# Kernel tuning notes

Measured on AMD Instinct MI355X. Metric: run time of the kernel, lower is better.

Reference implementation:

```python
import jax, jax.numpy as jnp
import numpy as np

B, T, N, D, H = 8, 24, 512, 128, 8
HD = D // H
HID = int(D * 2.0)
SCALES = (1.0, 0.01)


def _l2norm(a):
    # F.normalize(dim=-1), eps=1e-12
    n = jnp.sqrt(jnp.sum(a * a, axis=-1, keepdims=True))
    return a / jnp.maximum(n, 1e-12)


def _layernorm(a, g, b):
    mu = a.mean(-1, keepdims=True)
    var = ((a - mu) ** 2).mean(-1, keepdims=True)
    return (a - mu) / jnp.sqrt(var + 1e-5) * g + b


def _fast_attention_layer(z, qkv_w, out_w, out_b):
    # z: [B,T,N,D]; qkv_w: [D,3D]; out_w: [2D,D]; out_b: [D]
    b, t, n, d = z.shape
    q, k, v = jnp.split(z @ qkv_w, 3, axis=-1)          # each [B,T,N,D]
    q = q.reshape(b, t, n, H, HD)
    k = k.reshape(b, t, n, H, HD)
    v = v.reshape(b, t, n, H, HD)
    qn = _l2norm(q)
    kn = _l2norm(k)
    # spatial linear attention (tokens = nodes, axis 2)
    kvs = jnp.einsum('btnhm,btnhd->bthmd', kn, v)
    num = jnp.einsum('btnhm,bthmd->btnhd', qn, kvs) + n * v
    den = jnp.einsum('btnhm,bthm->btnh', qn, kn.sum(axis=2))[..., None] + n
    out_s = (num / den).reshape(b, t, n, d)
    # temporal linear attention (tokens = time steps, axis 1)
    kvt = jnp.einsum('btnhm,btnhd->bnhmd', kn, v)
    numt = jnp.einsum('btnhm,bnhmd->btnhd', qn, kvt) + t * v
    dent = jnp.einsum('btnhm,bnhm->btnh', qn, kn.sum(axis=1))[..., None] + t
    out_t = (numt / dent).reshape(b, t, n, d)
    return jnp.concatenate([out_s, out_t], axis=-1) @ out_w + out_b


def setup_inputs() -> dict:
    key = jax.random.key(0)
    ks = jax.random.split(key, 20)
    s = 0.02
    inp = {
        'x': jax.random.normal(ks[0], (B, T, N, D), jnp.float32),
        'graph': jax.random.uniform(ks[1], (T, N, N), jnp.float32) / N,
        'qkv_w0': jax.random.normal(ks[2], (D, 3 * D), jnp.float32) * s,
        'out_w0': jax.random.normal(ks[3], (2 * D, D), jnp.float32) * s,
        'out_b0': jnp.zeros((D,), jnp.float32),
        'pw_w0': jax.random.normal(ks[4], (D, D), jnp.float32) * s,
        'pw_b0': jax.random.normal(ks[5], (D,), jnp.float32) * s,
        'qkv_w1': jax.random.normal(ks[6], (D, 3 * D), jnp.float32) * s,
        'out_w1': jax.random.normal(ks[7], (2 * D, D), jnp.float32) * s,
        'out_b1': jnp.zeros((D,), jnp.float32),
        'pw_w1': jax.random.normal(ks[8], (D, D), jnp.float32) * s,
        'pw_b1': jax.random.normal(ks[9], (D,), jnp.float32) * s,
        'fc1_w': jax.random.normal(ks[10], (D, HID), jnp.float32) * s,
        'fc1_b': jnp.zeros((HID,), jnp.float32),
        'fc2_w': jax.random.normal(ks[11], (HID, D), jnp.float32) * s,
        'fc2_b': jnp.zeros((D,), jnp.float32),
        'ln1_g': jnp.ones((D,), jnp.float32),
        'ln1_b': jnp.zeros((D,), jnp.float32),
        'ln2_g': jnp.ones((D,), jnp.float32),
        'ln2_b': jnp.zeros((D,), jnp.float32),
    }
    return inp


def reference(x, graph, qkv_w0, out_w0, out_b0, pw_w0, pw_b0,
              qkv_w1, out_w1, out_b1, pw_w1, pw_b1,
              fc1_w, fc1_b, fc2_w, fc2_b, ln1_g, ln1_b, ln2_g, ln2_b):
    # GraphPropagate (Ks=order=2): x_loc = [x, graph @ x]; dropout in eval mode
    x1 = jnp.einsum('tni,btid->btnd', graph, x)
    x_loc = (x, x1)
    layer_params = ((qkv_w0, out_w0, out_b0, pw_w0, pw_b0),
                    (qkv_w1, out_w1, out_b1, pw_w1, pw_b1))
    c = x
    x_glo = x
    for k in range(2):
        qkv_w, out_w, out_b, pw_w, pw_b = layer_params[k]
        att = _fast_attention_layer(x_loc[k], qkv_w, out_w, out_b)
        pw = c @ pw_w + pw_b
        x_glo = x_glo + att * pw * SCALES[k]
        c = att
    h = _layernorm(x + x_glo, ln1_g, ln1_b)
    mlp = jax.nn.relu(h @ fc1_w + fc1_b) @ fc2_w + fc2_b
    return _layernorm(h + mlp, ln2_g, ln2_b)
```

## Files before the change

### kernel.cpp

```cpp
#include <hip/hip_runtime.h>
#include <cstddef>

#define Bb 8
#define Tt 24
#define Nn 512
#define Dd 128
#define Hh 8

typedef unsigned short u16;
using short8 = __attribute__((ext_vector_type(8))) short;
using f32x4  = __attribute__((ext_vector_type(4))) float;

__device__ __forceinline__ float b2f(u16 u) {
  union { unsigned u; float f; } w; w.u = ((unsigned)u) << 16; return w.f;
}
__device__ __forceinline__ u16 f2b(float f) {
  union { float f; unsigned u; } w; w.f = f;
  unsigned r = w.u + 0x7FFFu + ((w.u >> 16) & 1u);
  return (u16)(r >> 16);
}

__device__ __forceinline__ void mm_phase(const u16* __restrict__ A,
                                         const u16* __restrict__ BT,
                                         int K, int m0,
                                         u16* sA, u16* sB, f32x4 acc[4][4])
{
  const int tid = threadIdx.x;
  const int l = tid & 63, wid = tid >> 6;
  const int wm = (wid >> 1) << 6, wn = (wid & 1) << 6;
  int a_off[4], b_off[4];
#pragma unroll
  for (int i = 0; i < 4; ++i) {
    int ra = wm + i * 16 + (l & 15);
    a_off[i] = ((ra << 6) + ((l >> 4) << 4)) ^ ((ra & 7) << 4);
    int rb = wn + i * 16 + (l & 15);
    b_off[i] = ((rb << 6) + ((l >> 4) << 4)) ^ ((rb & 7) << 4);
  }
  const int r0 = tid >> 2, s0 = tid & 3;
  const int r1 = r0 + 64;
  const int w0 = ((r0 << 6) + (s0 << 4)) ^ ((r0 & 7) << 4);
  const int w1 = ((r1 << 6) + (s0 << 4)) ^ ((r1 & 7) << 4);
  const size_t aR0 = (size_t)(m0 + r0) * K, aR1 = (size_t)(m0 + r1) * K;
  const size_t bR0 = (size_t)r0 * K, bR1 = (size_t)r1 * K;
  const int ks = s0 * 8;
  for (int k0 = 0; k0 < K; k0 += 32) {
    short8 a0 = *(const short8*)(A + aR0 + k0 + ks);
    short8 a1 = *(const short8*)(A + aR1 + k0 + ks);
    short8 b0 = *(const short8*)(BT + bR0 + k0 + ks);
    short8 b1 = *(const short8*)(BT + bR1 + k0 + ks);
    __syncthreads();
    *(short8*)((char*)sA + w0) = a0;
    *(short8*)((char*)sA + w1) = a1;
    *(short8*)((char*)sB + w0) = b0;
    *(short8*)((char*)sB + w1) = b1;
    __syncthreads();
    short8 af[4], bf_[4];
#pragma unroll
    for (int i = 0; i < 4; ++i) {
      af[i]  = *(const short8*)((const char*)sA + a_off[i]);
      bf_[i] = *(const short8*)((const char*)sB + b_off[i]);
    }
#pragma unroll
    for (int mi = 0; mi < 4; ++mi)
#pragma unroll
      for (int ni = 0; ni < 4; ++ni)
        acc[mi][ni] = __builtin_amdgcn_mfma_f32_16x16x32_bf16(
            af[mi], bf_[ni], acc[mi][ni], 0, 0, 0);
  }
}

template <int OUTBF16, int RELU>
__device__ __forceinline__ void gemm_mfma_body(
    const u16* __restrict__ A, const u16* __restrict__ BT,
    const float* __restrict__ bias, void* __restrict__ Cv,
    int N, int K, int m0, int n0)
{
  __shared__ u16 sA[4096];
  __shared__ u16 sB[4096];
  f32x4 acc[4][4] = {};
  mm_phase(A, BT + (size_t)n0 * K, K, m0, sA, sB, acc);
  const int l = threadIdx.x & 63, wid = threadIdx.x >> 6;
  const int wm = (wid >> 1) << 6, wn = (wid & 1) << 6;
  const int cr = (l >> 4) << 2, cc = l & 15;
#pragma unroll
  for (int mi = 0; mi < 4; ++mi) {
    int rowb = m0 + wm + mi * 16 + cr;
#pragma unroll
    for (int ni = 0; ni < 4; ++ni) {
      int col = n0 + wn + ni * 16 + cc;
      float bb = bias ? bias[col] : 0.f;
#pragma unroll
      for (int r = 0; r < 4; ++r) {
        float v = acc[mi][ni][r] + bb;
        if (RELU) v = fmaxf(v, 0.f);
        size_t idx = (size_t)(rowb + r) * N + col;
        if (OUTBF16) ((u16*)Cv)[idx] = f2b(v);
        else         ((float*)Cv)[idx] = v;
      }
    }
  }
}

template <int OUTBF16, int RELU>
__global__ __launch_bounds__(256) void gemm_mfma_k(
    const u16* __restrict__ A, const u16* __restrict__ BT,
    const float* __restrict__ bias, void* __restrict__ C, int N, int K)
{
  gemm_mfma_body<OUTBF16, RELU>(A, BT, bias, C, N, K,
                                blockIdx.y * 128, blockIdx.x * 128);
}

__global__ __launch_bounds__(256) void gemm_mfma_graph(
    const u16* __restrict__ g, const u16* __restrict__ xT, u16* __restrict__ x1)
{
  const int bt = blockIdx.z, t = bt % Tt;
  gemm_mfma_body<1, 0>(g + (size_t)t * Nn * Nn, xT + (size_t)bt * Dd * Nn,
                       nullptr, x1 + (size_t)bt * Nn * Dd,
                       Dd, Nn, blockIdx.y * 128, 0);
}

__global__ __launch_bounds__(256) void gemm_og0(
    const u16* __restrict__ cat, const u16* __restrict__ outT, const float* __restrict__ ob,
    const u16* __restrict__ xb,  const u16* __restrict__ pwT,  const float* __restrict__ pb,
    const float* __restrict__ x, float* __restrict__ glo, u16* __restrict__ att0)
{
  __shared__ u16 sA[4096], sB[4096];
  const int m0 = blockIdx.x * 128;
  f32x4 accP[4][4] = {};
  mm_phase(xb, pwT, 128, m0, sA, sB, accP);
  f32x4 accO[4][4] = {};
  mm_phase(cat, outT, 256, m0, sA, sB, accO);
  const int l = threadIdx.x & 63, wid = threadIdx.x >> 6;
  const int wm = (wid >> 1) << 6, wn = (wid & 1) << 6;
  const int cr = (l >> 4) << 2, cc = l & 15;
#pragma unroll
  for (int mi = 0; mi < 4; ++mi) {
    int rowb = m0 + wm + mi * 16 + cr;
#pragma unroll
    for (int ni = 0; ni < 4; ++ni) {
      int col = wn + ni * 16 + cc;
      float obv = ob[col], pbv = pb[col];
#pragma unroll
      for (int r = 0; r < 4; ++r) {
        size_t idx = (size_t)(rowb + r) * 128 + col;
        float attv = accO[mi][ni][r] + obv;
        float pwv  = accP[mi][ni][r] + pbv;
        att0[idx] = f2b(attv);
        glo[idx] = x[idx] + attv * pwv;
      }
    }
  }
}

__global__ __launch_bounds__(256) void gemm_og1(
    const u16* __restrict__ cat, const u16* __restrict__ outT, const float* __restrict__ ob,
    const u16* __restrict__ att0, const u16* __restrict__ pwT, const float* __restrict__ pb,
    const float* __restrict__ glo, const float* __restrict__ x,
    const float* __restrict__ g, const float* __restrict__ be,
    u16* __restrict__ h16)
{
  __shared__ __align__(16) u16 smem[128 * 136];
  __shared__ float sg[128], sbt[128];
  u16* sA = smem;
  u16* sB = smem + 4096;
  if (threadIdx.x < 128) { sg[threadIdx.x] = g[threadIdx.x]; sbt[threadIdx.x] = be[threadIdx.x]; }
  const int m0 = blockIdx.x * 128;
  f32x4 accP[4][4] = {};
  mm_phase(att0, pwT, 128, m0, sA, sB, accP);
  f32x4 accO[4][4] = {};
  mm_phase(cat, outT, 256, m0, sA, sB, accO);
  const int l = threadIdx.x & 63, wid = threadIdx.x >> 6;
  const int wm = (wid >> 1) << 6, wn = (wid & 1) << 6;
  const int cr = (l >> 4) << 2, cc = l & 15;
  __syncthreads();
#pragma unroll
  for (int mi = 0; mi < 4; ++mi) {
    int lrow = wm + mi * 16 + cr;
#pragma unroll
    for (int ni = 0; ni < 4; ++ni) {
      int col = wn + ni * 16 + cc;
      float obv = ob[col], pbv = pb[col];
#pragma unroll
      for (int r = 0; r < 4; ++r) {
        size_t idx = (size_t)(m0 + lrow + r) * 128 + col;
        float attv = accO[mi][ni][r] + obv;
        float pwv  = accP[mi][ni][r] + pbv;
        float hpre = x[idx] + glo[idx] + attv * pwv * 0.01f;
        smem[(lrow + r) * 136 + col] = f2b(hpre);
      }
    }
  }
  __syncthreads();
  const int row = threadIdx.x >> 1, half = threadIdx.x & 1;
  const u16* rp = smem + row * 136 + half * 64;
  float s = 0.f, ss = 0.f;
#pragma unroll
  for (int j8 = 0; j8 < 8; ++j8) {
    short8 v = *(const short8*)(rp + j8 * 8);
#pragma unroll
    for (int j = 0; j < 8; ++j) { float f = b2f((u16)v[j]); s += f; ss += f * f; }
  }
  s += __shfl_xor(s, 1);
  ss += __shfl_xor(ss, 1);
  float mu = s * (1.f / 128.f);
  float rstd = rsqrtf(ss * (1.f / 128.f) - mu * mu + 1e-5f);
  size_t gbase = (size_t)(m0 + row) * 128 + half * 64;
#pragma unroll
  for (int j8 = 0; j8 < 8; ++j8) {
    short8 v = *(const short8*)(rp + j8 * 8);
    short8 o;
#pragma unroll
    for (int j = 0; j < 8; ++j) {
      int col = half * 64 + j8 * 8 + j;
      o[j] = (short)f2b((b2f((u16)v[j]) - mu) * rstd * sg[col] + sbt[col]);
    }
    *(short8*)(h16 + gbase + j8 * 8) = o;
  }
}

__global__ __launch_bounds__(256) void gemm_fc2ln(
    const u16* __restrict__ hid, const u16* __restrict__ fc2T, const float* __restrict__ fb,
    const u16* __restrict__ h16, const float* __restrict__ g, const float* __restrict__ be,
    float* __restrict__ out)
{
  __shared__ __align__(16) u16 smem[128 * 136];
  __shared__ float sg[128], sbt[128];
  u16* sA = smem;
  u16* sB = smem + 4096;
  if (threadIdx.x < 128) { sg[threadIdx.x] = g[threadIdx.x]; sbt[threadIdx.x] = be[threadIdx.x]; }
  const int m0 = blockIdx.x * 128;
  f32x4 accO[4][4] = {};
  mm_phase(hid, fc2T, 256, m0, sA, sB, accO);
  const int l = threadIdx.x & 63, wid = threadIdx.x >> 6;
  const int wm = (wid >> 1) << 6, wn = (wid & 1) << 6;
  const int cr = (l >> 4) << 2, cc = l & 15;
  __syncthreads();
#pragma unroll
  for (int mi = 0; mi < 4; ++mi) {
    int lrow = wm + mi * 16 + cr;
#pragma unroll
    for (int ni = 0; ni < 4; ++ni) {
      int col = wn + ni * 16 + cc;
      float fbv = fb[col];
#pragma unroll
      for (int r = 0; r < 4; ++r) {
        size_t idx = (size_t)(m0 + lrow + r) * 128 + col;
        float hpre = b2f(h16[idx]) + accO[mi][ni][r] + fbv;
        smem[(lrow + r) * 136 + col] = f2b(hpre);
      }
    }
  }
  __syncthreads();
  const int row = threadIdx.x >> 1, half = threadIdx.x & 1;
  const u16* rp = smem + row * 136 + half * 64;
  float s = 0.f, ss = 0.f;
#pragma unroll
  for (int j8 = 0; j8 < 8; ++j8) {
    short8 v = *(const short8*)(rp + j8 * 8);
#pragma unroll
    for (int j = 0; j < 8; ++j) { float f = b2f((u16)v[j]); s += f; ss += f * f; }
  }
  s += __shfl_xor(s, 1);
  ss += __shfl_xor(ss, 1);
  float mu = s * (1.f / 128.f);
  float rstd = rsqrtf(ss * (1.f / 128.f) - mu * mu + 1e-5f);
  size_t gbase = (size_t)(m0 + row) * 128 + half * 64;
#pragma unroll
  for (int j8 = 0; j8 < 8; ++j8) {
    short8 v = *(const short8*)(rp + j8 * 8);
    float4 o0, o1;
#pragma unroll
    for (int j = 0; j < 8; ++j) {
      int col = half * 64 + j8 * 8 + j;
      float y = (b2f((u16)v[j]) - mu) * rstd * sg[col] + sbt[col];
      if (j < 4) ((float*)&o0)[j] = y; else ((float*)&o1)[j - 4] = y;
    }
    *(float4*)(out + gbase + j8 * 8) = o0;
    *(float4*)(out + gbase + j8 * 8 + 4) = o1;
  }
}

__global__ __launch_bounds__(256) void qknorm(const u16* __restrict__ qkv,
                                              float* __restrict__ inv, size_t nidx)
{
  size_t idx = (size_t)blockIdx.x * 256 + threadIdx.x;
  if (idx >= nidx) return;
  size_t row = idx >> 4;
  int g = (int)(idx & 15);
  const u16* p = qkv + row * 384 + g * 16;
  short8 a = *(const short8*)p;
  short8 b = *(const short8*)(p + 8);
  float ss = 0.f;
#pragma unroll
  for (int j = 0; j < 8; ++j) {
    float f0 = b2f((u16)a[j]), f1 = b2f((u16)b[j]);
    ss += f0 * f0 + f1 * f1;
  }
  inv[idx] = 1.f / fmaxf(sqrtf(ss), 1e-12f);
}

__global__ __launch_bounds__(256) void cvt_f32_bf16(const float* __restrict__ src,
                                                    u16* __restrict__ dst, size_t n8)
{
  size_t i = (size_t)blockIdx.x * 256 + threadIdx.x;
  if (i >= n8) return;
  const float4* s = (const float4*)src;
  float4 u = s[i * 2], v = s[i * 2 + 1];
  short8 o;
  o[0] = (short)f2b(u.x); o[1] = (short)f2b(u.y);
  o[2] = (short)f2b(u.z); o[3] = (short)f2b(u.w);
  o[4] = (short)f2b(v.x); o[5] = (short)f2b(v.y);
  o[6] = (short)f2b(v.z); o[7] = (short)f2b(v.w);
  *(short8*)(dst + i * 8) = o;
}

__global__ __launch_bounds__(256) void transpose_cvt(const float* __restrict__ src,
                                                     u16* __restrict__ dst,
                                                     int R, int C)
{
  __shared__ u16 tile[64][65];
  const int tid = threadIdx.x;
  src += (size_t)blockIdx.z * R * C;
  dst += (size_t)blockIdx.z * R * C;
  const int c0 = blockIdx.x * 64, r0 = blockIdx.y * 64;
  const int tx = tid & 63, ty = tid >> 6;
#pragma unroll
  for (int i = 0; i < 64; i += 4)
    tile[ty + i][tx] = f2b(src[(size_t)(r0 + ty + i) * C + c0 + tx]);
  __syncthreads();
#pragma unroll
  for (int i = 0; i < 64; i += 4)
    dst[(size_t)(c0 + ty + i) * R + r0 + tx] = tile[tx][ty + i];
}

__global__ __launch_bounds__(256) void cvt_transpose_x(const float* __restrict__ src,
                                                       u16* __restrict__ xb,
                                                       u16* __restrict__ xT)
{
  __shared__ u16 tile[64][65];
  const int tid = threadIdx.x;
  const size_t zo = (size_t)blockIdx.z * Nn * Dd;
  src += zo; xb += zo; xT += zo;
  const int c0 = blockIdx.x * 64, r0 = blockIdx.y * 64;
  const int tx = tid & 63, ty = tid >> 6;
#pragma unroll
  for (int i = 0; i < 64; i += 4) {
    u16 b = f2b(src[(size_t)(r0 + ty + i) * Dd + c0 + tx]);
    tile[ty + i][tx] = b;
    xb[(size_t)(r0 + ty + i) * Dd + c0 + tx] = b;
  }
  __syncthreads();
#pragma unroll
  for (int i = 0; i < 64; i += 4)
    xT[(size_t)(c0 + ty + i) * Nn + r0 + tx] = tile[tx][ty + i];
}

__global__ __launch_bounds__(256) void spatial_stats(const u16* __restrict__ qkv,
                                                     const float* __restrict__ qkn,
                                                     float* __restrict__ kvs,
                                                     float* __restrict__ ksum)
{
  __shared__ u16 sKT[16 * 512];
  __shared__ u16 sVT[16 * 512];
  __shared__ float red[4][16][16];
  __shared__ float red2[4][16];
  const int bt = blockIdx.x, h = blockIdx.y;
  const int tid = threadIdx.x;

  u16 kr[2][16], vr[2][16];
#pragma unroll
  for (int r = 0; r < 2; ++r) {
    int n = tid * 2 + r;
    size_t rowg = (size_t)bt * 512 + n;
    size_t base = rowg * 384;
    float inv = qkn[rowg * 16 + 8 + h];
    short8 k0 = *(const short8*)(qkv + base + 128 + h * 16);
    short8 k1 = *(const short8*)(qkv + base + 136 + h * 16);
    short8 v0 = *(const short8*)(qkv + base + 256 + h * 16);
    short8 v1 = *(const short8*)(qkv + base + 264 + h * 16);
#pragma unroll
    for (int j = 0; j < 8; ++j) {
      kr[r][j]     = f2b(b2f((u16)k0[j]) * inv);
      kr[r][j + 8] = f2b(b2f((u16)k1[j]) * inv);
      vr[r][j] = (u16)v0[j]; vr[r][j + 8] = (u16)v1[j];
    }
  }
#pragma unroll
  for (int m = 0; m < 16; ++m) {
    unsigned pk = (unsigned)kr[0][m] | ((unsigned)kr[1][m] << 16);
    unsigned pv = (unsigned)vr[0][m] | ((unsigned)vr[1][m] << 16);
    int wa = ((m << 10) + (tid << 2)) ^ ((m & 7) << 4);
    *(unsigned*)((char*)sKT + wa) = pk;
    *(unsigned*)((char*)sVT + wa) = pv;
  }
  __syncthreads();

  const int l = tid & 63, w = tid >> 6;
  const int fr = l & 15, tq = l >> 4;
  short8 ones;
#pragma unroll
  for (int j = 0; j < 8; ++j) ones[j] = (short)0x3F80;
  f32x4 acc = {}, acs = {};
#pragma unroll
  for (int kk = 0; kk < 4; ++kk) {
    int noff = w * 128 + kk * 32 + tq * 8;
    int ra = ((fr << 10) + (noff << 1)) ^ ((fr & 7) << 4);
    short8 afr = *(const short8*)((const char*)sKT + ra);
    short8 bfr = *(const short8*)((const char*)sVT + ra);
    acc = __builtin_amdgcn_mfma_f32_16x16x32_bf16(afr, bfr, acc, 0, 0, 0);
    acs = __builtin_amdgcn_mfma_f32_16x16x32_bf16(afr, ones, acs, 0, 0, 0);
  }
#pragma unroll
  for (int r = 0; r < 4; ++r) red[w][tq * 4 + r][fr] = acc[r];
  if (fr == 0) {
#pragma unroll
    for (int r = 0; r < 4; ++r) red2[w][tq * 4 + r] = acs[r];
  }
  __syncthreads();
  const size_t o = (size_t)bt * 8 + h;
  {
    int m = tid >> 4, d = tid & 15;
    float s = red[0][m][d] + red[1][m][d] + red[2][m][d] + red[3][m][d];
    kvs[o * 256 + m * 16 + d] = s;
  }
  if (tid < 16) {
    float s = red2[0][tid] + red2[1][tid] + red2[2][tid] + red2[3][tid];
    ksum[o * 16 + tid] = s;
  }
}

__global__ __launch_bounds__(256) void temporal_stats(const u16* __restrict__ qkv,
                                                      const float* __restrict__ qkn,
                                                      float* __restrict__ kvt,
                                                      float* __restrict__ kst)
{
  __shared__ u16 sKT[128 * 32];
  __shared__ u16 sVT[128 * 32];
  const int nn = blockIdx.x, b = blockIdx.y;
  const int tid = threadIdx.x;
  if (tid < 128) {
    short8 z = {};
    int wa = ((tid << 6) + 48) ^ ((tid & 3) << 4);
    *(short8*)((char*)sKT + wa) = z;
    *(short8*)((char*)sVT + wa) = z;
  }
  for (int idx = tid; idx < 384; idx += 256) {
    int t = idx >> 4, c8 = idx & 15;
    size_t rowg = ((size_t)(b * 24 + t) * 512) + nn;
    float inv = qkn[rowg * 16 + 8 + (c8 >> 1)];
    short8 kv = *(const short8*)(qkv + rowg * 384 + 128 + c8 * 8);
    short8 vv = *(const short8*)(qkv + rowg * 384 + 256 + c8 * 8);
#pragma unroll
    for (int j = 0; j < 8; ++j) {
      int c = c8 * 8 + j;
      int wa = ((c << 6) + (t << 1)) ^ ((c & 3) << 4);
      *(u16*)((char*)sKT + wa) = f2b(b2f((u16)kv[j]) * inv);
      *(u16*)((char*)sVT + wa) = (u16)vv[j];
    }
  }
  __syncthreads();
  const int l = tid & 63, w = tid >> 6;
  const int fr = l & 15, tq = l >> 4;
  const size_t nb = (size_t)b * 512 + nn;
  short8 ones;
#pragma unroll
  for (int j = 0; j < 8; ++j) ones[j] = (short)0x3F80;
#pragma unroll
  for (int hi = 0; hi < 2; ++hi) {
    int h = w * 2 + hi;
    int c = h * 16 + fr;
    int ra = ((c << 6) + (tq << 4)) ^ ((c & 3) << 4);
    short8 afr = *(const short8*)((const char*)sKT + ra);
    short8 bfr = *(const short8*)((const char*)sVT + ra);
    f32x4 z = {};
    f32x4 acc = __builtin_amdgcn_mfma_f32_16x16x32_bf16(afr, bfr, z, 0, 0, 0);
    f32x4 acs = __builtin_amdgcn_mfma_f32_16x16x32_bf16(afr, ones, z, 0, 0, 0);
#pragma unroll
    for (int r = 0; r < 4; ++r)
      kvt[nb * 2048 + (size_t)(tq * 4 + r) * 128 + h * 16 + fr] = acc[r];
    if (fr == 0) {
#pragma unroll
      for (int r = 0; r < 4; ++r)
        kst[(nb * 8 + h) * 16 + tq * 4 + r] = acs[r];
    }
  }
}

__global__ __launch_bounds__(256) void attn_apply(const u16* __restrict__ qkv,
                                                  const float* __restrict__ qkn,
                                                  const float* __restrict__ kvs,
                                                  const float* __restrict__ kss,
                                                  const float* __restrict__ kvt,
                                                  const float* __restrict__ kst,
                                                  u16* __restrict__ out_cat)
{
  __shared__ float s_kvt[2048];
  __shared__ float s_kst[8][16];
  const int nn = blockIdx.x, b = blockIdx.y;
  const int t0 = blockIdx.z * 8;
  const int tid = threadIdx.x;
  const size_t nb = (size_t)b * 512 + nn;
  for (int i = tid; i < 2048; i += 256) s_kvt[i] = kvt[nb * 2048 + i];
  if (tid < 128) s_kst[tid >> 4][tid & 15] = kst[nb * 128 + tid];
  __syncthreads();
  const int c = tid;
  const bool temporal = c >= 128;
  const int cl = c & 127;
  const int hh = cl >> 4, d = c & 15;
  const float cnt = temporal ? 24.f : 512.f;
  for (int t = t0; t < t0 + 8; ++t) {
    const size_t row = ((size_t)(b * 24 + t) * 512) + nn;
    const u16* qp = qkv + row * 384 + hh * 16;
    short8 q0 = *(const short8*)qp;
    short8 q1 = *(const short8*)(qp + 8);
    const float inv = qkn[row * 16 + hh];
    float qf[16];
#pragma unroll
    for (int j = 0; j < 8; ++j) {
      qf[j] = b2f((u16)q0[j]);
      qf[j + 8] = b2f((u16)q1[j]);
    }
    float acc = 0.f, dp;
    if (temporal) {
#pragma unroll
      for (int mI = 0; mI < 16; ++mI)
        acc = fmaf(qf[mI], s_kvt[mI * 128 + cl], acc);
      dp = qf[d] * s_kst[hh][d];
    } else {
      const float* Mm = kvs + ((size_t)(b * 24 + t) * 8 + hh) * 256;
      const float* Ks = kss + ((size_t)(b * 24 + t) * 8 + hh) * 16;
#pragma unroll
      for (int mI = 0; mI < 16; ++mI)
        acc = fmaf(qf[mI], Mm[mI * 16 + d], acc);
      dp = qf[d] * Ks[d];
    }
    dp += __shfl_xor(dp, 1);
    dp += __shfl_xor(dp, 2);
    dp += __shfl_xor(dp, 4);
    dp += __shfl_xor(dp, 8);
    float vv = b2f(qkv[row * 384 + 256 + cl]);
    out_cat[row * 256 + c] = f2b((acc * inv + cnt * vv) / (dp * inv + cnt));
  }
}

extern "C" void kernel_launch(void* const* d_in, const int* in_sizes, int n_in,
                              void* d_out, int out_size, void* d_ws, size_t ws_size,
                              hipStream_t stream)
{
  const float* x      = (const float*)d_in[0];
  const float* graph  = (const float*)d_in[1];
  const float* qkv_w0 = (const float*)d_in[2];
  const float* out_w0 = (const float*)d_in[3];
  const float* out_b0 = (const float*)d_in[4];
  const float* pw_w0  = (const float*)d_in[5];
  const float* pw_b0  = (const float*)d_in[6];
  const float* qkv_w1 = (const float*)d_in[7];
  const float* out_w1 = (const float*)d_in[8];
  const float* out_b1 = (const float*)d_in[9];
  const float* pw_w1  = (const float*)d_in[10];
  const float* pw_b1  = (const float*)d_in[11];
  const float* fc1_w  = (const float*)d_in[12];
  const float* fc1_b  = (const float*)d_in[13];
  const float* fc2_w  = (const float*)d_in[14];
  const float* fc2_b  = (const float*)d_in[15];
  const float* ln1_g  = (const float*)d_in[16];
  const float* ln1_b  = (const float*)d_in[17];
  const float* ln2_g  = (const float*)d_in[18];
  const float* ln2_b  = (const float*)d_in[19];
  float* out = (float*)d_out;

  auto al = [](size_t v) { return (v + 255) & ~(size_t)255; };
  const size_t Rb = 12288;
  const size_t fixed = al((size_t)Tt * Nn * Nn * 2) + 2 * al((size_t)384 * 128 * 2)
                     + 2 * al((size_t)128 * 256 * 2) + 2 * al((size_t)128 * 128 * 2)
                     + al((size_t)256 * 128 * 2) + al((size_t)128 * 256 * 2);
  const size_t perb = al(Rb * 768) + al(Rb * 512) + 4 * al(Rb * 256) + al(Rb * 512)
                    + al(Rb * 64)
                    + al((size_t)Tt * 8 * 256 * 4) + al((size_t)Tt * 8 * 16 * 4)
                    + al((size_t)Nn * 8 * 256 * 4) + al((size_t)Nn * 8 * 16 * 4);
  int CB = 8;
  while (CB > 1 && fixed + (size_t)CB * perb > ws_size) CB >>= 1;
  const size_t Mc = (size_t)CB * Rb;

  char* cur = (char*)d_ws;
  auto alloc = [&](size_t bytes) { char* p = cur; cur += (bytes + 255) & ~(size_t)255; return p; };
  u16* g_b16 = (u16*)alloc((size_t)Tt * Nn * Nn * 2);
  u16* qkvT0 = (u16*)alloc((size_t)384 * 128 * 2);
  u16* qkvT1 = (u16*)alloc((size_t)384 * 128 * 2);
  u16* outT0 = (u16*)alloc((size_t)128 * 256 * 2);
  u16* outT1 = (u16*)alloc((size_t)128 * 256 * 2);
  u16* pwT0  = (u16*)alloc((size_t)128 * 128 * 2);
  u16* pwT1  = (u16*)alloc((size_t)128 * 128 * 2);
  u16* fc1T  = (u16*)alloc((size_t)256 * 128 * 2);
  u16* fc2T  = (u16*)alloc((size_t)128 * 256 * 2);
  u16* qkvb  = (u16*)alloc(Mc * 768);
  u16* catb  = (u16*)alloc(Mc * 512);
  u16* x1b   = (u16*)alloc(Mc * 256);
  u16* att0  = (u16*)alloc(Mc * 256);
  u16* xb    = (u16*)alloc(Mc * 256);
  u16* xT    = (u16*)alloc(Mc * 256);
  float* glo = (float*)alloc(Mc * 512);
  float* qkn = (float*)alloc(Mc * 64);
  float* kvs = (float*)alloc((size_t)CB * Tt * 8 * 256 * 4);
  float* kss = (float*)alloc((size_t)CB * Tt * 8 * 16 * 4);
  float* kvt = (float*)alloc((size_t)CB * Nn * 8 * 256 * 4);
  float* kst = (float*)alloc((size_t)CB * Nn * 8 * 16 * 4);

  dim3 blk(256);
  cvt_f32_bf16<<<dim3((Tt * Nn * Nn / 8 + 255) / 256), blk, 0, stream>>>(
      graph, g_b16, (size_t)Tt * Nn * Nn / 8);
  transpose_cvt<<<dim3(6, 2, 1), blk, 0, stream>>>(qkv_w0, qkvT0, 128, 384);
  transpose_cvt<<<dim3(6, 2, 1), blk, 0, stream>>>(qkv_w1, qkvT1, 128, 384);
  transpose_cvt<<<dim3(2, 4, 1), blk, 0, stream>>>(out_w0, outT0, 256, 128);
  transpose_cvt<<<dim3(2, 4, 1), blk, 0, stream>>>(out_w1, outT1, 256, 128);
  transpose_cvt<<<dim3(2, 2, 1), blk, 0, stream>>>(pw_w0, pwT0, 128, 128);
  transpose_cvt<<<dim3(2, 2, 1), blk, 0, stream>>>(pw_w1, pwT1, 128, 128);
  transpose_cvt<<<dim3(4, 2, 1), blk, 0, stream>>>(fc1_w, fc1T, 128, 256);
  transpose_cvt<<<dim3(2, 4, 1), blk, 0, stream>>>(fc2_w, fc2T, 256, 128);

  const int MB = (int)(Mc / 128);
  const int nchunk = Bb / CB;
  for (int c = 0; c < nchunk; ++c) {
    const size_t off = (size_t)c * Mc * 128;
    const float* xc = x + off;
    float* outc = out + off;

    cvt_transpose_x<<<dim3(2, 8, CB * Tt), blk, 0, stream>>>(xc, xb, xT);
    gemm_mfma_graph<<<dim3(1, 4, CB * Tt), blk, 0, stream>>>(g_b16, xT, x1b);

    gemm_mfma_k<1, 0><<<dim3(3, MB), blk, 0, stream>>>(xb, qkvT0, nullptr, qkvb, 384, 128);
    qknorm<<<dim3((unsigned)(Mc / 16)), blk, 0, stream>>>(qkvb, qkn, Mc * 16);
    spatial_stats<<<dim3(CB * Tt, Hh), blk, 0, stream>>>(qkvb, qkn, kvs, kss);
    temporal_stats<<<dim3(Nn, CB), blk, 0, stream>>>(qkvb, qkn, kvt, kst);
    attn_apply<<<dim3(Nn, CB, 3), blk, 0, stream>>>(qkvb, qkn, kvs, kss, kvt, kst, catb);
    gemm_og0<<<dim3(MB), blk, 0, stream>>>(catb, outT0, out_b0, xb, pwT0, pw_b0,
                                           xc, glo, att0);

    gemm_mfma_k<1, 0><<<dim3(3, MB), blk, 0, stream>>>(x1b, qkvT1, nullptr, qkvb, 384, 128);
    qknorm<<<dim3((unsigned)(Mc / 16)), blk, 0, stream>>>(qkvb, qkn, Mc * 16);
    spatial_stats<<<dim3(CB * Tt, Hh), blk, 0, stream>>>(qkvb, qkn, kvs, kss);
    temporal_stats<<<dim3(Nn, CB), blk, 0, stream>>>(qkvb, qkn, kvt, kst);
    attn_apply<<<dim3(Nn, CB, 3), blk, 0, stream>>>(qkvb, qkn, kvs, kss, kvt, kst, catb);
    u16* h16 = qkvb;
    gemm_og1<<<dim3(MB), blk, 0, stream>>>(catb, outT1, out_b1, att0, pwT1, pw_b1,
                                           glo, xc, ln1_g, ln1_b, h16);

    gemm_mfma_k<1, 1><<<dim3(2, MB), blk, 0, stream>>>(h16, fc1T, fc1_b, catb, 256, 128);
    gemm_fc2ln<<<dim3(MB), blk, 0, stream>>>(catb, fc2T, fc2_b, h16, ln2_g, ln2_b, outc);
  }

  (void)in_sizes; (void)n_in; (void)out_size;
}
```

Before: 657.5 us.

## Store layer-0 gated term in bf16, transpose kvs, and restructure attn_apply per node pair

gemm_og0 no longer reads x or writes an fp32 glo buffer. It stores only att0*pw0 in bf16, and gemm_og1 rebuilds the pre-norm sum as 2x + gp0 + scaled term, which cuts fp32 traffic at some precision cost. spatial_stats now writes kvs transposed so attn_apply can load each column as four float4 vectors. attn_apply now gives each thread both the spatial and the temporal output for one channel, with two nodes per block, removing the branch and halving the grid.

```diff
diff --git a/kernel.cpp b/kernel.cpp
--- a/kernel.cpp
+++ b/kernel.cpp
@@ -122,7 +122,7 @@
 __global__ __launch_bounds__(256) void gemm_og0(
     const u16* __restrict__ cat, const u16* __restrict__ outT, const float* __restrict__ ob,
     const u16* __restrict__ xb,  const u16* __restrict__ pwT,  const float* __restrict__ pb,
-    const float* __restrict__ x, float* __restrict__ glo, u16* __restrict__ att0)
+    u16* __restrict__ gp0, u16* __restrict__ att0)
 {
   __shared__ u16 sA[4096], sB[4096];
   const int m0 = blockIdx.x * 128;
@@ -146,7 +146,7 @@
         float attv = accO[mi][ni][r] + obv;
         float pwv  = accP[mi][ni][r] + pbv;
         att0[idx] = f2b(attv);
-        glo[idx] = x[idx] + attv * pwv;
+        gp0[idx] = f2b(attv * pwv);
       }
     }
   }
@@ -155,7 +155,7 @@
 __global__ __launch_bounds__(256) void gemm_og1(
     const u16* __restrict__ cat, const u16* __restrict__ outT, const float* __restrict__ ob,
     const u16* __restrict__ att0, const u16* __restrict__ pwT, const float* __restrict__ pb,
-    const float* __restrict__ glo, const float* __restrict__ x,
+    const u16* __restrict__ gp0, const float* __restrict__ x,
     const float* __restrict__ g, const float* __restrict__ be,
     u16* __restrict__ h16)
 {
@@ -185,7 +185,7 @@
         size_t idx = (size_t)(m0 + lrow + r) * 128 + col;
         float attv = accO[mi][ni][r] + obv;
         float pwv  = accP[mi][ni][r] + pbv;
-        float hpre = x[idx] + glo[idx] + attv * pwv * 0.01f;
+        float hpre = 2.f * x[idx] + b2f(gp0[idx]) + attv * pwv * 0.01f;
         smem[(lrow + r) * 136 + col] = f2b(hpre);
       }
     }
@@ -357,7 +357,7 @@
 
 __global__ __launch_bounds__(256) void spatial_stats(const u16* __restrict__ qkv,
                                                      const float* __restrict__ qkn,
-                                                     float* __restrict__ kvs,
+                                                     float* __restrict__ kvs2,
                                                      float* __restrict__ ksum)
 {
   __shared__ u16 sKT[16 * 512];
@@ -421,7 +421,7 @@
   {
     int m = tid >> 4, d = tid & 15;
     float s = red[0][m][d] + red[1][m][d] + red[2][m][d] + red[3][m][d];
-    kvs[o * 256 + m * 16 + d] = s;
+    kvs2[o * 256 + d * 16 + m] = s;
   }
   if (tid < 16) {
     float s = red2[0][tid] + red2[1][tid] + red2[2][tid] + red2[3][tid];
@@ -488,26 +488,23 @@
 
 __global__ __launch_bounds__(256) void attn_apply(const u16* __restrict__ qkv,
                                                   const float* __restrict__ qkn,
-                                                  const float* __restrict__ kvs,
+                                                  const float* __restrict__ kvs2,
                                                   const float* __restrict__ kss,
                                                   const float* __restrict__ kvt,
                                                   const float* __restrict__ kst,
                                                   u16* __restrict__ out_cat)
 {
-  __shared__ float s_kvt[2048];
-  __shared__ float s_kst[8][16];
-  const int nn = blockIdx.x, b = blockIdx.y;
+  __shared__ float s_kvt[2][2048];
+  const int nn0 = blockIdx.x * 2, b = blockIdx.y;
   const int t0 = blockIdx.z * 8;
   const int tid = threadIdx.x;
+  const int sub = tid >> 7, cl = tid & 127;
+  const int nn = nn0 + sub;
   const size_t nb = (size_t)b * 512 + nn;
-  for (int i = tid; i < 2048; i += 256) s_kvt[i] = kvt[nb * 2048 + i];
-  if (tid < 128) s_kst[tid >> 4][tid & 15] = kst[nb * 128 + tid];
-  __syncthreads();
-  const int c = tid;
-  const bool temporal = c >= 128;
-  const int cl = c & 127;
-  const int hh = cl >> 4, d = c & 15;
-  const float cnt = temporal ? 24.f : 512.f;
+  for (int i = cl; i < 2048; i += 128) s_kvt[sub][i] = kvt[nb * 2048 + i];
+  __syncthreads();
+  const int hh = cl >> 4, d = cl & 15;
+  const float kst_d = kst[(nb * 8 + hh) * 16 + d];
   for (int t = t0; t < t0 + 8; ++t) {
     const size_t row = ((size_t)(b * 24 + t) * 512) + nn;
     const u16* qp = qkv + row * 384 + hh * 16;
@@ -520,26 +517,30 @@
       qf[j] = b2f((u16)q0[j]);
       qf[j + 8] = b2f((u16)q1[j]);
     }
-    float acc = 0.f, dp;
-    if (temporal) {
-#pragma unroll
-      for (int mI = 0; mI < 16; ++mI)
-        acc = fmaf(qf[mI], s_kvt[mI * 128 + cl], acc);
-      dp = qf[d] * s_kst[hh][d];
-    } else {
-      const float* Mm = kvs + ((size_t)(b * 24 + t) * 8 + hh) * 256;
-      const float* Ks = kss + ((size_t)(b * 24 + t) * 8 + hh) * 16;
-#pragma unroll
-      for (int mI = 0; mI < 16; ++mI)
-        acc = fmaf(qf[mI], Mm[mI * 16 + d], acc);
-      dp = qf[d] * Ks[d];
-    }
-    dp += __shfl_xor(dp, 1);
-    dp += __shfl_xor(dp, 2);
-    dp += __shfl_xor(dp, 4);
-    dp += __shfl_xor(dp, 8);
+    const size_t sbase = ((size_t)(b * 24 + t) * 8 + hh) * 256 + d * 16;
+    const float4* M4 = (const float4*)(kvs2 + sbase);
+    float4 m0 = M4[0], m1 = M4[1], m2 = M4[2], m3 = M4[3];
+    float accs = qf[0] * m0.x + qf[1] * m0.y + qf[2] * m0.z + qf[3] * m0.w;
+    accs = fmaf(qf[4], m1.x, fmaf(qf[5], m1.y, fmaf(qf[6], m1.z, fmaf(qf[7], m1.w, accs))));
+    accs = fmaf(qf[8], m2.x, fmaf(qf[9], m2.y, fmaf(qf[10], m2.z, fmaf(qf[11], m2.w, accs))));
+    accs = fmaf(qf[12], m3.x, fmaf(qf[13], m3.y, fmaf(qf[14], m3.z, fmaf(qf[15], m3.w, accs))));
+    float dps = qf[d] * kss[((size_t)(b * 24 + t) * 8 + hh) * 16 + d];
+    dps += __shfl_xor(dps, 1);
+    dps += __shfl_xor(dps, 2);
+    dps += __shfl_xor(dps, 4);
+    dps += __shfl_xor(dps, 8);
+    float acct = 0.f;
+#pragma unroll
+    for (int mI = 0; mI < 16; ++mI)
+      acct = fmaf(qf[mI], s_kvt[sub][mI * 128 + cl], acct);
+    float dpt = qf[d] * kst_d;
+    dpt += __shfl_xor(dpt, 1);
+    dpt += __shfl_xor(dpt, 2);
+    dpt += __shfl_xor(dpt, 4);
+    dpt += __shfl_xor(dpt, 8);
     float vv = b2f(qkv[row * 384 + 256 + cl]);
-    out_cat[row * 256 + c] = f2b((acc * inv + cnt * vv) / (dp * inv + cnt));
+    out_cat[row * 256 + cl]       = f2b((accs * inv + 512.f * vv) / (dps * inv + 512.f));
+    out_cat[row * 256 + 128 + cl] = f2b((acct * inv + 24.f * vv) / (dpt * inv + 24.f));
   }
 }
 
@@ -599,7 +600,7 @@
   u16* att0  = (u16*)alloc(Mc * 256);
   u16* xb    = (u16*)alloc(Mc * 256);
   u16* xT    = (u16*)alloc(Mc * 256);
-  float* glo = (float*)alloc(Mc * 512);
+  u16* gp0   = (u16*)alloc(Mc * 512);
   float* qkn = (float*)alloc(Mc * 64);
   float* kvs = (float*)alloc((size_t)CB * Tt * 8 * 256 * 4);
   float* kss = (float*)alloc((size_t)CB * Tt * 8 * 16 * 4);
@@ -632,18 +633,18 @@
     qknorm<<<dim3((unsigned)(Mc / 16)), blk, 0, stream>>>(qkvb, qkn, Mc * 16);
     spatial_stats<<<dim3(CB * Tt, Hh), blk, 0, stream>>>(qkvb, qkn, kvs, kss);
     temporal_stats<<<dim3(Nn, CB), blk, 0, stream>>>(qkvb, qkn, kvt, kst);
-    attn_apply<<<dim3(Nn, CB, 3), blk, 0, stream>>>(qkvb, qkn, kvs, kss, kvt, kst, catb);
+    attn_apply<<<dim3(Nn / 2, CB, 3), blk, 0, stream>>>(qkvb, qkn, kvs, kss, kvt, kst, catb);
     gemm_og0<<<dim3(MB), blk, 0, stream>>>(catb, outT0, out_b0, xb, pwT0, pw_b0,
-                                           xc, glo, att0);
+                                           gp0, att0);
 
     gemm_mfma_k<1, 0><<<dim3(3, MB), blk, 0, stream>>>(x1b, qkvT1, nullptr, qkvb, 384, 128);
     qknorm<<<dim3((unsigned)(Mc / 16)), blk, 0, stream>>>(qkvb, qkn, Mc * 16);
     spatial_stats<<<dim3(CB * Tt, Hh), blk, 0, stream>>>(qkvb, qkn, kvs, kss);
     temporal_stats<<<dim3(Nn, CB), blk, 0, stream>>>(qkvb, qkn, kvt, kst);
-    attn_apply<<<dim3(Nn, CB, 3), blk, 0, stream>>>(qkvb, qkn, kvs, kss, kvt, kst, catb);
+    attn_apply<<<dim3(Nn / 2, CB, 3), blk, 0, stream>>>(qkvb, qkn, kvs, kss, kvt, kst, catb);
     u16* h16 = qkvb;
     gemm_og1<<<dim3(MB), blk, 0, stream>>>(catb, outT1, out_b1, att0, pwT1, pw_b1,
-                                           glo, xc, ln1_g, ln1_b, h16);
+                                           gp0, xc, ln1_g, ln1_b, h16);
 
     gemm_mfma_k<1, 1><<<dim3(2, MB), blk, 0, stream>>>(h16, fc1T, fc1_b, catb, 256, 128);
     gemm_fc2ln<<<dim3(MB), blk, 0, stream>>>(catb, fc2T, fc2_b, h16, ln2_g, ln2_b, outc);
```

New measurement: 658.0 us. No clear change (+0.1%).

## Double GEMM K-step to 64 and store layer-0 gated term in bf16

Applied to the files above, without the earlier changes.

The shared MFMA main loop now stages 64-wide K slices (twice the LDS tile) per barrier pair, halving the number of synchronisation rounds and issuing more loads per iteration. Separately, gemm_og0 no longer reads x and writes an fp32 x_glo accumulator. It writes only att*pw as bf16, and gemm_og1 reconstructs 2x + that term, which cuts global traffic. The trade-offs are larger LDS use per block, which may lower occupancy, and reduced precision on the intermediate gated term.

```diff
diff --git a/kernel.cpp b/kernel.cpp
--- a/kernel.cpp
+++ b/kernel.cpp
@@ -28,44 +28,53 @@
   const int tid = threadIdx.x;
   const int l = tid & 63, wid = tid >> 6;
   const int wm = (wid >> 1) << 6, wn = (wid & 1) << 6;
-  int a_off[4], b_off[4];
-#pragma unroll
-  for (int i = 0; i < 4; ++i) {
-    int ra = wm + i * 16 + (l & 15);
-    a_off[i] = ((ra << 6) + ((l >> 4) << 4)) ^ ((ra & 7) << 4);
-    int rb = wn + i * 16 + (l & 15);
-    b_off[i] = ((rb << 6) + ((l >> 4) << 4)) ^ ((rb & 7) << 4);
-  }
-  const int r0 = tid >> 2, s0 = tid & 3;
-  const int r1 = r0 + 64;
-  const int w0 = ((r0 << 6) + (s0 << 4)) ^ ((r0 & 7) << 4);
-  const int w1 = ((r1 << 6) + (s0 << 4)) ^ ((r1 & 7) << 4);
-  const size_t aR0 = (size_t)(m0 + r0) * K, aR1 = (size_t)(m0 + r1) * K;
-  const size_t bR0 = (size_t)r0 * K, bR1 = (size_t)r1 * K;
-  const int ks = s0 * 8;
-  for (int k0 = 0; k0 < K; k0 += 32) {
-    short8 a0 = *(const short8*)(A + aR0 + k0 + ks);
-    short8 a1 = *(const short8*)(A + aR1 + k0 + ks);
-    short8 b0 = *(const short8*)(BT + bR0 + k0 + ks);
-    short8 b1 = *(const short8*)(BT + bR1 + k0 + ks);
+  int a_off[2][4], b_off[2][4];
+#pragma unroll
+  for (int kk = 0; kk < 2; ++kk)
+#pragma unroll
+    for (int i = 0; i < 4; ++i) {
+      int ra = wm + i * 16 + (l & 15);
+      a_off[kk][i] = ((ra << 7) + (kk << 6) + ((l >> 4) << 4)) ^ ((ra & 7) << 4);
+      int rb = wn + i * 16 + (l & 15);
+      b_off[kk][i] = ((rb << 7) + (kk << 6) + ((l >> 4) << 4)) ^ ((rb & 7) << 4);
+    }
+  const int srow = tid >> 3, schunk = tid & 7;
+  int w_off[4];
+#pragma unroll
+  for (int j = 0; j < 4; ++j) {
+    int r = srow + j * 32;
+    w_off[j] = ((r << 7) + (schunk << 4)) ^ ((r & 7) << 4);
+  }
+  const int ke = schunk * 8;
+  for (int k0 = 0; k0 < K; k0 += 64) {
+    short8 a[4], b[4];
+#pragma unroll
+    for (int j = 0; j < 4; ++j) {
+      a[j] = *(const short8*)(A + (size_t)(m0 + srow + j * 32) * K + k0 + ke);
+      b[j] = *(const short8*)(BT + (size_t)(srow + j * 32) * K + k0 + ke);
+    }
     __syncthreads();
-    *(short8*)((char*)sA + w0) = a0;
-    *(short8*)((char*)sA + w1) = a1;
-    *(short8*)((char*)sB + w0) = b0;
-    *(short8*)((char*)sB + w1) = b1;
+#pragma unroll
+    for (int j = 0; j < 4; ++j) {
+      *(short8*)((char*)sA + w_off[j]) = a[j];
+      *(short8*)((char*)sB + w_off[j]) = b[j];
+    }
     __syncthreads();
-    short8 af[4], bf_[4];
-#pragma unroll
-    for (int i = 0; i < 4; ++i) {
-      af[i]  = *(const short8*)((const char*)sA + a_off[i]);
-      bf_[i] = *(const short8*)((const char*)sB + b_off[i]);
-    }
-#pragma unroll
-    for (int mi = 0; mi < 4; ++mi)
-#pragma unroll
-      for (int ni = 0; ni < 4; ++ni)
-        acc[mi][ni] = __builtin_amdgcn_mfma_f32_16x16x32_bf16(
-            af[mi], bf_[ni], acc[mi][ni], 0, 0, 0);
+#pragma unroll
+    for (int kk = 0; kk < 2; ++kk) {
+      short8 af[4], bf_[4];
+#pragma unroll
+      for (int i = 0; i < 4; ++i) {
+        af[i]  = *(const short8*)((const char*)sA + a_off[kk][i]);
+        bf_[i] = *(const short8*)((const char*)sB + b_off[kk][i]);
+      }
+#pragma unroll
+      for (int mi = 0; mi < 4; ++mi)
+#pragma unroll
+        for (int ni = 0; ni < 4; ++ni)
+          acc[mi][ni] = __builtin_amdgcn_mfma_f32_16x16x32_bf16(
+              af[mi], bf_[ni], acc[mi][ni], 0, 0, 0);
+    }
   }
 }
 
@@ -75,8 +84,8 @@
     const float* __restrict__ bias, void* __restrict__ Cv,
     int N, int K, int m0, int n0)
 {
-  __shared__ u16 sA[4096];
-  __shared__ u16 sB[4096];
+  __shared__ u16 sA[8192];
+  __shared__ u16 sB[8192];
   f32x4 acc[4][4] = {};
   mm_phase(A, BT + (size_t)n0 * K, K, m0, sA, sB, acc);
   const int l = threadIdx.x & 63, wid = threadIdx.x >> 6;
@@ -122,9 +131,9 @@
 __global__ __launch_bounds__(256) void gemm_og0(
     const u16* __restrict__ cat, const u16* __restrict__ outT, const float* __restrict__ ob,
     const u16* __restrict__ xb,  const u16* __restrict__ pwT,  const float* __restrict__ pb,
-    const float* __restrict__ x, float* __restrict__ glo, u16* __restrict__ att0)
-{
-  __shared__ u16 sA[4096], sB[4096];
+    u16* __restrict__ gp0, u16* __restrict__ att0)
+{
+  __shared__ u16 sA[8192], sB[8192];
   const int m0 = blockIdx.x * 128;
   f32x4 accP[4][4] = {};
   mm_phase(xb, pwT, 128, m0, sA, sB, accP);
@@ -146,7 +155,7 @@
         float attv = accO[mi][ni][r] + obv;
         float pwv  = accP[mi][ni][r] + pbv;
         att0[idx] = f2b(attv);
-        glo[idx] = x[idx] + attv * pwv;
+        gp0[idx] = f2b(attv * pwv);
       }
     }
   }
@@ -155,14 +164,14 @@
 __global__ __launch_bounds__(256) void gemm_og1(
     const u16* __restrict__ cat, const u16* __restrict__ outT, const float* __restrict__ ob,
     const u16* __restrict__ att0, const u16* __restrict__ pwT, const float* __restrict__ pb,
-    const float* __restrict__ glo, const float* __restrict__ x,
+    const u16* __restrict__ gp0, const float* __restrict__ x,
     const float* __restrict__ g, const float* __restrict__ be,
     u16* __restrict__ h16)
 {
   __shared__ __align__(16) u16 smem[128 * 136];
   __shared__ float sg[128], sbt[128];
   u16* sA = smem;
-  u16* sB = smem + 4096;
+  u16* sB = smem + 8192;
   if (threadIdx.x < 128) { sg[threadIdx.x] = g[threadIdx.x]; sbt[threadIdx.x] = be[threadIdx.x]; }
   const int m0 = blockIdx.x * 128;
   f32x4 accP[4][4] = {};
@@ -185,7 +194,7 @@
         size_t idx = (size_t)(m0 + lrow + r) * 128 + col;
         float attv = accO[mi][ni][r] + obv;
         float pwv  = accP[mi][ni][r] + pbv;
-        float hpre = x[idx] + glo[idx] + attv * pwv * 0.01f;
+        float hpre = 2.f * x[idx] + b2f(gp0[idx]) + attv * pwv * 0.01f;
         smem[(lrow + r) * 136 + col] = f2b(hpre);
       }
     }
@@ -226,7 +235,7 @@
   __shared__ __align__(16) u16 smem[128 * 136];
   __shared__ float sg[128], sbt[128];
   u16* sA = smem;
-  u16* sB = smem + 4096;
+  u16* sB = smem + 8192;
   if (threadIdx.x < 128) { sg[threadIdx.x] = g[threadIdx.x]; sbt[threadIdx.x] = be[threadIdx.x]; }
   const int m0 = blockIdx.x * 128;
   f32x4 accO[4][4] = {};
@@ -599,7 +608,7 @@
   u16* att0  = (u16*)alloc(Mc * 256);
   u16* xb    = (u16*)alloc(Mc * 256);
   u16* xT    = (u16*)alloc(Mc * 256);
-  float* glo = (float*)alloc(Mc * 512);
+  u16* gp0   = (u16*)alloc(Mc * 512);
   float* qkn = (float*)alloc(Mc * 64);
   float* kvs = (float*)alloc((size_t)CB * Tt * 8 * 256 * 4);
   float* kss = (float*)alloc((size_t)CB * Tt * 8 * 16 * 4);
@@ -634,7 +643,7 @@
     temporal_stats<<<dim3(Nn, CB), blk, 0, stream>>>(qkvb, qkn, kvt, kst);
     attn_apply<<<dim3(Nn, CB, 3), blk, 0, stream>>>(qkvb, qkn, kvs, kss, kvt, kst, catb);
     gemm_og0<<<dim3(MB), blk, 0, stream>>>(catb, outT0, out_b0, xb, pwT0, pw_b0,
-                                           xc, glo, att0);
+                                           gp0, att0);
 
     gemm_mfma_k<1, 0><<<dim3(3, MB), blk, 0, stream>>>(x1b, qkvT1, nullptr, qkvb, 384, 128);
     qknorm<<<dim3((unsigned)(Mc / 16)), blk, 0, stream>>>(qkvb, qkn, Mc * 16);
@@ -643,7 +652,7 @@
     attn_apply<<<dim3(Nn, CB, 3), blk, 0, stream>>>(qkvb, qkn, kvs, kss, kvt, kst, catb);
     u16* h16 = qkvb;
     gemm_og1<<<dim3(MB), blk, 0, stream>>>(catb, outT1, out_b1, att0, pwT1, pw_b1,
-                                           glo, xc, ln1_g, ln1_b, h16);
+                                           gp0, xc, ln1_g, ln1_b, h16);
 
     gemm_mfma_k<1, 1><<<dim3(2, MB), blk, 0, stream>>>(h16, fc1T, fc1_b, catb, 256, 128);
     gemm_fc2ln<<<dim3(MB), blk, 0, stream>>>(catb, fc2T, fc2_b, h16, ln2_g, ln2_b, outc);
```

New measurement: 630.2 us. 4.2% less time.
